# Optimization experiments

Hardware: AMD Instinct MI355X
Metric: run time of the kernel (lower is better)

Reference implementation:

```python
import jax, jax.numpy as jnp
import numpy as np

N, E, G = 100000, 400000, 2000
F_IN, HID, H = 74, 64, 4
HID4 = HID * H           # 256, per-node feature after flatten(1)
POOL = 3 * HID4          # 768, concat(mean, max, sum)
OUT = 128
NEG_SLOPE = 0.2          # DGL GATConv default LeakyReLU slope


def setup_inputs() -> dict:
    key = jax.random.key(0)
    ks = jax.random.split(key, 20)
    p = lambda k, shape: (jax.random.normal(k, shape, jnp.float32) * 0.05)
    inp = {
        "node_feat": jax.random.normal(ks[0], (N, F_IN), jnp.float32),
        "src": jax.random.randint(ks[1], (E,), 0, N, jnp.int32),
        "dst": jax.random.randint(ks[2], (E,), 0, N, jnp.int32),
        # every graph gets exactly N//G nodes (sorted, non-empty segments)
        "graph_ids": jnp.arange(N, dtype=jnp.int32) // (N // G),
        "enc_W": p(ks[3], (F_IN, HID)), "enc_b": jnp.zeros((HID,), jnp.float32),
    }
    in_dims = [HID, HID4, HID4]
    for l in range(3):
        inp[f"W{l}"] = p(ks[4 + 4 * l], (in_dims[l], H * HID))
        inp[f"al{l}"] = p(ks[5 + 4 * l], (H, HID))
        inp[f"ar{l}"] = p(ks[6 + 4 * l], (H, HID))
        inp[f"b{l}"] = jnp.zeros((H * HID,), jnp.float32)
    inp["r1_W"] = p(ks[16], (POOL, HID)); inp["r1_b"] = jnp.zeros((HID,), jnp.float32)
    inp["r2_W"] = p(ks[17], (HID, OUT)); inp["r2_b"] = jnp.zeros((OUT,), jnp.float32)
    return inp


def _gat_layer(h, src, dst, W, al, ar, b):
    # DGL GATConv (eval mode: dropouts are identity), activation=ReLU
    z = (h @ W).reshape(N, H, HID)                       # [N,H,O]
    el = jnp.einsum("nho,ho->nh", z, al)                 # [N,H]
    er = jnp.einsum("nho,ho->nh", z, ar)
    e = jax.nn.leaky_relu(el[src] + er[dst], NEG_SLOPE)  # [E,H]
    # segment softmax over incoming edges of each dst node, per head
    m = jax.ops.segment_max(e, dst, num_segments=N)      # [N,H]
    ex = jnp.exp(e - m[dst])
    s = jax.ops.segment_sum(ex, dst, num_segments=N)     # [N,H]
    a = ex / s[dst]                                      # [E,H]
    out = jax.ops.segment_sum(z[src] * a[:, :, None], dst, num_segments=N)
    out = out + b.reshape(1, H, HID)                     # GATConv bias
    return jax.nn.relu(out).reshape(N, HID4)             # flatten(1)


def reference(node_feat, src, dst, graph_ids, enc_W, enc_b,
              W0, al0, ar0, b0, W1, al1, ar1, b1, W2, al2, ar2, b2,
              r1_W, r1_b, r2_W, r2_b):
    h = node_feat @ enc_W + enc_b                        # node encoder
    h = _gat_layer(h, src, dst, W0, al0, ar0, b0)
    h = _gat_layer(h, src, dst, W1, al1, ar1, b1)
    h = _gat_layer(h, src, dst, W2, al2, ar2, b2)
    # multi-pool readout: mean / max / sum over nodes of each graph
    h_sum = jax.ops.segment_sum(h, graph_ids, num_segments=G)
    cnt = jax.ops.segment_sum(jnp.ones((N, 1), h.dtype), graph_ids, num_segments=G)
    h_mean = h_sum / cnt
    h_max = jax.ops.segment_max(h, graph_ids, num_segments=G)
    hg = jnp.concatenate([h_mean, h_max, h_sum], axis=1)  # [G, 3*HID4]
    hg = jax.nn.relu(hg @ r1_W + r1_b)
    return hg @ r2_W + r2_b                              # [G, OUT]
```

## Files before the change

kernel.cpp:

```cpp
#include <hip/hip_runtime.h>

#define N_NODES 100000
#define N_EDGES 400000
#define N_GRAPHS 2000
#define F_IN 74
#define ENC_KP 96
#define HID 64
#define NHEAD 4
#define HID4 256
#define OUT_DIM 128
#define NODES_PER_G 50

typedef __attribute__((ext_vector_type(8))) short short8;
typedef __attribute__((ext_vector_type(4))) float f32x4;

__device__ inline ushort f2bf(float f) {
  union { float f; unsigned u; } v; v.f = f;
  unsigned u = v.u;
  return (ushort)((u + 0x7FFFu + ((u >> 16) & 1u)) >> 16);
}
__device__ inline float bf2f(ushort b) {
  union { unsigned u; float f; } v; v.u = ((unsigned)b) << 16;
  return v.f;
}
__device__ inline float leaky(float x) { return x >= 0.f ? x : 0.2f * x; }

__device__ inline void glds16(const ushort* g, ushort* l) {
  __builtin_amdgcn_global_load_lds(
      (const __attribute__((address_space(1))) void*)g,
      (__attribute__((address_space(3))) void*)l, 16, 0, 0);
}

__global__ __launch_bounds__(256) void k_count(const int* __restrict__ dst,
                                               int* __restrict__ off) {
  int e = blockIdx.x * 256 + threadIdx.x;
  if (e < N_EDGES) atomicAdd(&off[dst[e] + 1], 1);
}

__global__ __launch_bounds__(256) void k_scan1(int* __restrict__ data, int n,
                                               int* __restrict__ blksum) {
  __shared__ int sh[256];
  int t = threadIdx.x;
  int base = blockIdx.x * 1024 + t * 4;
  int v0 = (base + 0 < n) ? data[base + 0] : 0;
  int v1 = (base + 1 < n) ? data[base + 1] : 0;
  int v2 = (base + 2 < n) ? data[base + 2] : 0;
  int v3 = (base + 3 < n) ? data[base + 3] : 0;
  v1 += v0; v2 += v1; v3 += v2;
  int tot = v3;
  sh[t] = tot;
  __syncthreads();
  for (int o = 1; o < 256; o <<= 1) {
    int x = (t >= o) ? sh[t - o] : 0;
    __syncthreads();
    sh[t] += x;
    __syncthreads();
  }
  int excl = sh[t] - tot;
  if (base + 0 < n) data[base + 0] = v0 + excl;
  if (base + 1 < n) data[base + 1] = v1 + excl;
  if (base + 2 < n) data[base + 2] = v2 + excl;
  if (base + 3 < n) data[base + 3] = v3 + excl;
  if (t == 255) blksum[blockIdx.x] = sh[255];
}

__global__ __launch_bounds__(256) void k_scan2(int* __restrict__ blksum, int nb) {
  __shared__ int sh[256];
  int t = threadIdx.x;
  sh[t] = (t < nb) ? blksum[t] : 0;
  __syncthreads();
  for (int o = 1; o < 256; o <<= 1) {
    int x = (t >= o) ? sh[t - o] : 0;
    __syncthreads();
    sh[t] += x;
    __syncthreads();
  }
  if (t < nb) blksum[t] = sh[t];
}

__global__ __launch_bounds__(256) void k_scan3(int* __restrict__ data, int n,
                                               const int* __restrict__ blksum) {
  int b = blockIdx.x;
  if (b == 0) return;
  int add = blksum[b - 1];
  int base = b * 1024 + threadIdx.x * 4;
  for (int j = 0; j < 4; ++j)
    if (base + j < n) data[base + j] += add;
}

__global__ __launch_bounds__(256) void k_scatter(const int* __restrict__ dst,
                                                 const int* __restrict__ src,
                                                 const int* __restrict__ off,
                                                 int* __restrict__ cursor,
                                                 int* __restrict__ srcs) {
  int e = blockIdx.x * 256 + threadIdx.x;
  if (e >= N_EDGES) return;
  int d = dst[e];
  int pos = off[d] + atomicAdd(&cursor[d], 1);
  srcs[pos] = src[e];
}

__global__ __launch_bounds__(256) void k_sortseg(const int* __restrict__ off,
                                                 int* __restrict__ srcs) {
  int n = blockIdx.x * 256 + threadIdx.x;
  if (n >= N_NODES) return;
  int beg = off[n], end = off[n + 1];
  for (int i = beg + 1; i < end; ++i) {
    int key = srcs[i];
    int j = i - 1;
    while (j >= beg && srcs[j] > key) { srcs[j + 1] = srcs[j]; --j; }
    srcs[j + 1] = key;
  }
}

__global__ __launch_bounds__(256) void k_pad_nf(const float* __restrict__ nf,
                                                ushort* __restrict__ nfb) {
  long long idx = (long long)blockIdx.x * 256 + threadIdx.x;
  if (idx >= (long long)N_NODES * ENC_KP) return;
  int n = (int)(idx / ENC_KP);
  int c = (int)(idx - (long long)n * ENC_KP);
  ushort v = 0;
  if (c < F_IN) v = f2bf(nf[(size_t)n * F_IN + c]);
  nfb[idx] = v;
}

__global__ __launch_bounds__(256) void k_wt_enc(const float* __restrict__ W,
                                                ushort* __restrict__ Wte) {
  int idx = blockIdx.x * 256 + threadIdx.x;
  if (idx >= HID * ENC_KP) return;
  int col = idx / ENC_KP;
  int k = idx - col * ENC_KP;
  ushort v = 0;
  if (k < F_IN) v = f2bf(W[(size_t)k * HID + col]);
  Wte[idx] = v;
}

__global__ __launch_bounds__(256) void k_enc_mfma(const ushort* __restrict__ A,
                                                  const ushort* __restrict__ Bt,
                                                  const float* __restrict__ bias,
                                                  ushort* __restrict__ Cb) {
  __shared__ ushort As[128][104];
  __shared__ ushort Bs[64][104];
  int t = threadIdx.x;
  int lane = t & 63;
  int wid = t >> 6;
  int brow = blockIdx.x * 128;

  {
    int r = t >> 1;
    int o = (t & 1) * 48;
    int gr = brow + r;
    const ushort* srcp = A + (size_t)gr * ENC_KP + o;
#pragma unroll
    for (int i = 0; i < 6; ++i) {
      int4 v = make_int4(0, 0, 0, 0);
      if (gr < N_NODES) v = *(const int4*)(srcp + i * 8);
      *(int4*)&As[r][o + i * 8] = v;
    }
  }
  if (t < 128) {
    int r = t >> 1;
    int o = (t & 1) * 48;
#pragma unroll
    for (int i = 0; i < 6; ++i)
      *(int4*)&Bs[r][o + i * 8] = *(const int4*)(Bt + (size_t)r * ENC_KP + o + i * 8);
  }
  __syncthreads();

  int fr = lane & 15;
  int ko = (lane >> 4) * 8;
  f32x4 acc[2][4];
#pragma unroll
  for (int m = 0; m < 2; ++m)
#pragma unroll
    for (int n = 0; n < 4; ++n) acc[m][n] = (f32x4)(0.f);

#pragma unroll
  for (int ks = 0; ks < 3; ++ks) {
    short8 a[2], b[4];
#pragma unroll
    for (int m = 0; m < 2; ++m) a[m] = *(const short8*)&As[wid * 32 + m * 16 + fr][ks * 32 + ko];
#pragma unroll
    for (int n = 0; n < 4; ++n) b[n] = *(const short8*)&Bs[n * 16 + fr][ks * 32 + ko];
#pragma unroll
    for (int m = 0; m < 2; ++m)
#pragma unroll
      for (int n = 0; n < 4; ++n)
        acc[m][n] = __builtin_amdgcn_mfma_f32_16x16x32_bf16(a[m], b[n], acc[m][n], 0, 0, 0);
  }

  int r0 = (lane >> 4) * 4;
  int cc = lane & 15;
#pragma unroll
  for (int m = 0; m < 2; ++m) {
#pragma unroll
    for (int j = 0; j < 4; ++j) {
      int row = brow + wid * 32 + m * 16 + r0 + j;
      if (row >= N_NODES) continue;
#pragma unroll
      for (int n = 0; n < 4; ++n) {
        int col = n * 16 + cc;
        Cb[(size_t)row * HID + col] = f2bf(acc[m][n][j] + bias[col]);
      }
    }
  }
}

template <int K>
__global__ __launch_bounds__(256) void k_wt(const float* __restrict__ W,
                                            ushort* __restrict__ Wt) {
  int idx = blockIdx.x * 256 + threadIdx.x;
  if (idx >= K * HID4) return;
  int k = idx >> 8;
  int n = idx & 255;
  Wt[(size_t)n * K + k] = f2bf(W[idx]);
}

template <int K>
__global__ __launch_bounds__(256) void k_gemm_mfma(const ushort* __restrict__ A,
                                                   const ushort* __restrict__ Bt,
                                                   ushort* __restrict__ Cb,
                                                   const float* __restrict__ al,
                                                   const float* __restrict__ ar,
                                                   float* __restrict__ el,
                                                   float* __restrict__ er,
                                                   int n_rows) {
  __shared__ __align__(16) ushort As[128 * 32];
  __shared__ __align__(16) ushort Bs[128 * 32];
  int t = threadIdx.x;
  int lane = t & 63;
  int wid = t >> 6;
  int wr = wid >> 1, wc = wid & 1;
  int brow = blockIdx.x * 128;
  int bcol = blockIdx.y * 128;

  f32x4 acc[4][4];
#pragma unroll
  for (int m = 0; m < 4; ++m)
#pragma unroll
    for (int n = 0; n < 4; ++n) acc[m][n] = (f32x4)(0.f);

  int srow0 = (wid * 2 + 0) * 16 + (lane >> 2);
  int srow1 = (wid * 2 + 1) * 16 + (lane >> 2);
  int skc = (lane & 3) * 8;
  int ga0 = brow + srow0; if (ga0 > n_rows - 1) ga0 = n_rows - 1;
  int ga1 = brow + srow1; if (ga1 > n_rows - 1) ga1 = n_rows - 1;
  const ushort* pa0 = A + (size_t)ga0 * K + skc;
  const ushort* pa1 = A + (size_t)ga1 * K + skc;
  const ushort* pb0 = Bt + (size_t)(bcol + srow0) * K + skc;
  const ushort* pb1 = Bt + (size_t)(bcol + srow1) * K + skc;
  ushort* la0 = As + (wid * 2 + 0) * 512;
  ushort* la1 = As + (wid * 2 + 1) * 512;
  ushort* lb0 = Bs + (wid * 2 + 0) * 512;
  ushort* lb1 = Bs + (wid * 2 + 1) * 512;

  int fr = lane & 15;
  int ko = (lane >> 4) * 8;

  for (int k0 = 0; k0 < K; k0 += 32) {
    glds16(pa0 + k0, la0);
    glds16(pa1 + k0, la1);
    glds16(pb0 + k0, lb0);
    glds16(pb1 + k0, lb1);
    __syncthreads();
    short8 a[4], b[4];
#pragma unroll
    for (int m = 0; m < 4; ++m)
      a[m] = *(const short8*)(As + (wr * 64 + m * 16 + fr) * 32 + ko);
#pragma unroll
    for (int n = 0; n < 4; ++n)
      b[n] = *(const short8*)(Bs + (wc * 64 + n * 16 + fr) * 32 + ko);
#pragma unroll
    for (int m = 0; m < 4; ++m)
#pragma unroll
      for (int n = 0; n < 4; ++n)
        acc[m][n] = __builtin_amdgcn_mfma_f32_16x16x32_bf16(a[m], b[n], acc[m][n], 0, 0, 0);
    __syncthreads();
  }

  int r0 = (lane >> 4) * 4;
  int cc = lane & 15;
  int q = blockIdx.y * 2 + wc;
  float alr[4], arr[4];
#pragma unroll
  for (int n = 0; n < 4; ++n) {
    int col = bcol + wc * 64 + n * 16 + cc;
    alr[n] = al[col];
    arr[n] = ar[col];
  }
#pragma unroll
  for (int m = 0; m < 4; ++m) {
#pragma unroll
    for (int j = 0; j < 4; ++j) {
      float pl = 0.f, pr = 0.f;
#pragma unroll
      for (int n = 0; n < 4; ++n) {
        pl = fmaf(acc[m][n][j], alr[n], pl);
        pr = fmaf(acc[m][n][j], arr[n], pr);
      }
#pragma unroll
      for (int o = 1; o < 16; o <<= 1) {
        pl += __shfl_xor(pl, o, 64);
        pr += __shfl_xor(pr, o, 64);
      }
      int row = brow + wr * 64 + m * 16 + r0 + j;
      if (row >= n_rows) continue;
      if (cc == 0) {
        el[(size_t)row * NHEAD + q] = pl;
        er[(size_t)row * NHEAD + q] = pr;
      }
#pragma unroll
      for (int n = 0; n < 4; ++n)
        Cb[(size_t)row * HID4 + bcol + wc * 64 + n * 16 + cc] = f2bf(acc[m][n][j]);
    }
  }
}

__global__ __launch_bounds__(256) void k_agg(const ushort* __restrict__ zb,
                                             const float* __restrict__ el,
                                             const float* __restrict__ er,
                                             const int* __restrict__ off,
                                             const int* __restrict__ srcs,
                                             const float* __restrict__ bias,
                                             ushort* __restrict__ outb) {
  int w = (blockIdx.x * 256 + threadIdx.x) >> 6;
  int lane = threadIdx.x & 63;
  int half = lane >> 5;
  int li = lane & 31;
  int n = w * 2 + half;
  if (n >= N_NODES) return;
  int h = li >> 3;
  int c = li * 8;
  int beg = off[n], end = off[n + 1];
  float erh = er[(size_t)n * NHEAD + h];

  float s = 0.f;
  float acc[8] = {0.f, 0.f, 0.f, 0.f, 0.f, 0.f, 0.f, 0.f};

  float e0 = 0.f, e1 = 0.f, e2 = 0.f;
  int4 z0 = make_int4(0, 0, 0, 0), z1 = z0, z2 = z0;
  if (beg < end) {
    int sn = srcs[beg];
    e0 = el[(size_t)sn * NHEAD + h];
    z0 = *(const int4*)(zb + (size_t)sn * HID4 + c);
  }
  if (beg + 1 < end) {
    int sn = srcs[beg + 1];
    e1 = el[(size_t)sn * NHEAD + h];
    z1 = *(const int4*)(zb + (size_t)sn * HID4 + c);
  }
  if (beg + 2 < end) {
    int sn = srcs[beg + 2];
    e2 = el[(size_t)sn * NHEAD + h];
    z2 = *(const int4*)(zb + (size_t)sn * HID4 + c);
  }
  for (int p = beg; p < end; ++p) {
    float ev = e0;
    int4 zv = z0;
    e0 = e1; z0 = z1;
    e1 = e2; z1 = z2;
    if (p + 3 < end) {
      int sn = srcs[p + 3];
      e2 = el[(size_t)sn * NHEAD + h];
      z2 = *(const int4*)(zb + (size_t)sn * HID4 + c);
    }
    float pv = __expf(leaky(ev + erh));
    s += pv;
    const ushort* us = (const ushort*)&zv;
#pragma unroll
    for (int j = 0; j < 8; ++j) acc[j] = fmaf(pv, bf2f(us[j]), acc[j]);
  }
  float inv = (s > 0.f) ? 1.f / s : 0.f;
  float4 b40 = *(const float4*)(bias + c);
  float4 b41 = *(const float4*)(bias + c + 4);
  float bb[8] = {b40.x, b40.y, b40.z, b40.w, b41.x, b41.y, b41.z, b41.w};
  int4 ov;
  ushort* os = (ushort*)&ov;
#pragma unroll
  for (int j = 0; j < 8; ++j) os[j] = f2bf(fmaxf(acc[j] * inv + bb[j], 0.f));
  *(int4*)(outb + (size_t)n * HID4 + c) = ov;
}

__global__ __launch_bounds__(256) void k_pool_mlp(const ushort* __restrict__ h,
                                                  const float* __restrict__ r1W,
                                                  const float* __restrict__ r1b,
                                                  const float* __restrict__ r2W,
                                                  const float* __restrict__ r2b,
                                                  float* __restrict__ out) {
  __shared__ float pooled[3 * HID4];
  __shared__ float part[4][HID];
  __shared__ float mid[HID];
  int g = blockIdx.x;
  int t = threadIdx.x;
  const ushort* base = h + (size_t)g * NODES_PER_G * HID4;
  float sum = 0.f, mx = -1e30f;
  for (int i = 0; i < NODES_PER_G; ++i) {
    float v = bf2f(base[(size_t)i * HID4 + t]);
    sum += v;
    mx = fmaxf(mx, v);
  }
  pooled[t] = sum / (float)NODES_PER_G;
  pooled[HID4 + t] = mx;
  pooled[2 * HID4 + t] = sum;
  __syncthreads();
  {
    int o = t & 63, chunk = t >> 6;
    float acc = 0.f;
    int k0 = chunk * 192;
    for (int k = k0; k < k0 + 192; ++k) acc = fmaf(pooled[k], r1W[k * HID + o], acc);
    part[chunk][o] = acc;
  }
  __syncthreads();
  if (t < HID) {
    float acc = r1b[t] + part[0][t] + part[1][t] + part[2][t] + part[3][t];
    mid[t] = fmaxf(acc, 0.f);
  }
  __syncthreads();
  if (t < OUT_DIM) {
    float acc = r2b[t];
    for (int k = 0; k < HID; ++k) acc = fmaf(mid[k], r2W[k * OUT_DIM + t], acc);
    out[(size_t)g * OUT_DIM + t] = acc;
  }
}

extern "C" void kernel_launch(void* const* d_in, const int* in_sizes, int n_in,
                              void* d_out, int out_size, void* d_ws, size_t ws_size,
                              hipStream_t stream) {
  const float* node_feat = (const float*)d_in[0];
  const int* src = (const int*)d_in[1];
  const int* dst = (const int*)d_in[2];
  const float* enc_W = (const float*)d_in[4];
  const float* enc_b = (const float*)d_in[5];
  const float* Wl[3] = {(const float*)d_in[6], (const float*)d_in[10], (const float*)d_in[14]};
  const float* all[3] = {(const float*)d_in[7], (const float*)d_in[11], (const float*)d_in[15]};
  const float* arl[3] = {(const float*)d_in[8], (const float*)d_in[12], (const float*)d_in[16]};
  const float* bl[3] = {(const float*)d_in[9], (const float*)d_in[13], (const float*)d_in[17]};
  const float* r1W = (const float*)d_in[18];
  const float* r1b = (const float*)d_in[19];
  const float* r2W = (const float*)d_in[20];
  const float* r2b = (const float*)d_in[21];
  float* out = (float*)d_out;

  char* p = (char*)d_ws;
  auto alloc = [&](size_t bytes) {
    void* r = (void*)p;
    p += (bytes + 255) & ~(size_t)255;
    return r;
  };
  int* off = (int*)alloc((N_NODES + 1) * sizeof(int));
  int* cursor = (int*)alloc(N_NODES * sizeof(int));
  int* srcs = (int*)alloc(N_EDGES * sizeof(int));
  int* blksum = (int*)alloc(256 * sizeof(int));
  float* el = (float*)alloc((size_t)N_NODES * NHEAD * sizeof(float));
  float* er = (float*)alloc((size_t)N_NODES * NHEAD * sizeof(float));
  ushort* Qb = (ushort*)alloc((size_t)N_NODES * HID4 * sizeof(ushort));
  ushort* Pb = (ushort*)alloc((size_t)N_NODES * HID4 * sizeof(ushort));
  ushort* Wt = (ushort*)alloc((size_t)HID4 * HID4 * sizeof(ushort));
  ushort* nfb = (ushort*)alloc((size_t)N_NODES * ENC_KP * sizeof(ushort));
  ushort* Wte = (ushort*)alloc((size_t)HID * ENC_KP * sizeof(ushort));

  hipMemsetAsync(off, 0, (N_NODES + 1) * sizeof(int), stream);
  hipMemsetAsync(cursor, 0, N_NODES * sizeof(int), stream);
  k_count<<<(N_EDGES + 255) / 256, 256, 0, stream>>>(dst, off);
  const int SCAN_N = N_NODES + 1;
  const int NB = (SCAN_N + 1023) / 1024;
  k_scan1<<<NB, 256, 0, stream>>>(off, SCAN_N, blksum);
  k_scan2<<<1, 256, 0, stream>>>(blksum, NB);
  k_scan3<<<NB, 256, 0, stream>>>(off, SCAN_N, blksum);
  k_scatter<<<(N_EDGES + 255) / 256, 256, 0, stream>>>(dst, src, off, cursor, srcs);
  k_sortseg<<<(N_NODES + 255) / 256, 256, 0, stream>>>(off, srcs);

  k_pad_nf<<<(int)(((long long)N_NODES * ENC_KP + 255) / 256), 256, 0, stream>>>(node_feat, nfb);
  k_wt_enc<<<(HID * ENC_KP + 255) / 256, 256, 0, stream>>>(enc_W, Wte);
  k_enc_mfma<<<(N_NODES + 127) / 128, 256, 0, stream>>>(nfb, Wte, enc_b, Pb);

  dim3 ggrid((N_NODES + 127) / 128, HID4 / 128);
  const int AGG_WAVES = (N_NODES + 1) / 2;
  const int AGG_BLOCKS = (AGG_WAVES + 3) / 4;
  for (int l = 0; l < 3; ++l) {
    if (l == 0) {
      k_wt<HID><<<(HID * HID4 + 255) / 256, 256, 0, stream>>>(Wl[0], Wt);
      k_gemm_mfma<HID><<<ggrid, 256, 0, stream>>>(Pb, Wt, Qb, all[0], arl[0], el, er, N_NODES);
    } else {
      k_wt<HID4><<<(HID4 * HID4 + 255) / 256, 256, 0, stream>>>(Wl[l], Wt);
      k_gemm_mfma<HID4><<<ggrid, 256, 0, stream>>>(Pb, Wt, Qb, all[l], arl[l], el, er, N_NODES);
    }
    k_agg<<<AGG_BLOCKS, 256, 0, stream>>>(Qb, el, er, off, srcs, bl[l], Pb);
  }

  k_pool_mlp<<<N_GRAPHS, 256, 0, stream>>>(Pb, r1W, r1b, r2W, r2b, out);
}
```

Before: 376.0 us.

## Fuse feature padding into encoder, double-buffer GEMM LDS, prefetch edge indices

```diff
diff --git a/kernel.cpp b/kernel.cpp
--- a/kernel.cpp
+++ b/kernel.cpp
@@ -113,17 +113,6 @@
   }
 }
 
-__global__ __launch_bounds__(256) void k_pad_nf(const float* __restrict__ nf,
-                                                ushort* __restrict__ nfb) {
-  long long idx = (long long)blockIdx.x * 256 + threadIdx.x;
-  if (idx >= (long long)N_NODES * ENC_KP) return;
-  int n = (int)(idx / ENC_KP);
-  int c = (int)(idx - (long long)n * ENC_KP);
-  ushort v = 0;
-  if (c < F_IN) v = f2bf(nf[(size_t)n * F_IN + c]);
-  nfb[idx] = v;
-}
-
 __global__ __launch_bounds__(256) void k_wt_enc(const float* __restrict__ W,
                                                 ushort* __restrict__ Wte) {
   int idx = blockIdx.x * 256 + threadIdx.x;
@@ -135,7 +124,7 @@
   Wte[idx] = v;
 }
 
-__global__ __launch_bounds__(256) void k_enc_mfma(const ushort* __restrict__ A,
+__global__ __launch_bounds__(256) void k_enc_mfma(const float* __restrict__ nf,
                                                   const ushort* __restrict__ Bt,
                                                   const float* __restrict__ bias,
                                                   ushort* __restrict__ Cb) {
@@ -146,17 +135,13 @@
   int wid = t >> 6;
   int brow = blockIdx.x * 128;
 
-  {
-    int r = t >> 1;
-    int o = (t & 1) * 48;
+  for (int i = t; i < 128 * ENC_KP; i += 256) {
+    int r = i / ENC_KP;
+    int c = i - r * ENC_KP;
     int gr = brow + r;
-    const ushort* srcp = A + (size_t)gr * ENC_KP + o;
-#pragma unroll
-    for (int i = 0; i < 6; ++i) {
-      int4 v = make_int4(0, 0, 0, 0);
-      if (gr < N_NODES) v = *(const int4*)(srcp + i * 8);
-      *(int4*)&As[r][o + i * 8] = v;
-    }
+    float v = 0.f;
+    if (gr < N_NODES && c < F_IN) v = nf[(size_t)gr * F_IN + c];
+    As[r][c] = f2bf(v);
   }
   if (t < 128) {
     int r = t >> 1;
@@ -225,8 +210,8 @@
                                                    float* __restrict__ el,
                                                    float* __restrict__ er,
                                                    int n_rows) {
-  __shared__ __align__(16) ushort As[128 * 32];
-  __shared__ __align__(16) ushort Bs[128 * 32];
+  __shared__ __align__(16) ushort As[2][128 * 32];
+  __shared__ __align__(16) ushort Bs[2][128 * 32];
   int t = threadIdx.x;
   int lane = t & 63;
   int wid = t >> 6;
@@ -249,33 +234,40 @@
   const ushort* pa1 = A + (size_t)ga1 * K + skc;
   const ushort* pb0 = Bt + (size_t)(bcol + srow0) * K + skc;
   const ushort* pb1 = Bt + (size_t)(bcol + srow1) * K + skc;
-  ushort* la0 = As + (wid * 2 + 0) * 512;
-  ushort* la1 = As + (wid * 2 + 1) * 512;
-  ushort* lb0 = Bs + (wid * 2 + 0) * 512;
-  ushort* lb1 = Bs + (wid * 2 + 1) * 512;
+  int lo0 = (wid * 2 + 0) * 512;
+  int lo1 = (wid * 2 + 1) * 512;
 
   int fr = lane & 15;
   int ko = (lane >> 4) * 8;
 
+  glds16(pa0, &As[0][lo0]);
+  glds16(pa1, &As[0][lo1]);
+  glds16(pb0, &Bs[0][lo0]);
+  glds16(pb1, &Bs[0][lo1]);
+  __syncthreads();
+  int cur = 0;
+
   for (int k0 = 0; k0 < K; k0 += 32) {
-    glds16(pa0 + k0, la0);
-    glds16(pa1 + k0, la1);
-    glds16(pb0 + k0, lb0);
-    glds16(pb1 + k0, lb1);
-    __syncthreads();
+    if (k0 + 32 < K) {
+      glds16(pa0 + k0 + 32, &As[cur ^ 1][lo0]);
+      glds16(pa1 + k0 + 32, &As[cur ^ 1][lo1]);
+      glds16(pb0 + k0 + 32, &Bs[cur ^ 1][lo0]);
+      glds16(pb1 + k0 + 32, &Bs[cur ^ 1][lo1]);
+    }
     short8 a[4], b[4];
 #pragma unroll
     for (int m = 0; m < 4; ++m)
-      a[m] = *(const short8*)(As + (wr * 64 + m * 16 + fr) * 32 + ko);
+      a[m] = *(const short8*)(&As[cur][0] + (wr * 64 + m * 16 + fr) * 32 + ko);
 #pragma unroll
     for (int n = 0; n < 4; ++n)
-      b[n] = *(const short8*)(Bs + (wc * 64 + n * 16 + fr) * 32 + ko);
+      b[n] = *(const short8*)(&Bs[cur][0] + (wc * 64 + n * 16 + fr) * 32 + ko);
 #pragma unroll
     for (int m = 0; m < 4; ++m)
 #pragma unroll
       for (int n = 0; n < 4; ++n)
         acc[m][n] = __builtin_amdgcn_mfma_f32_16x16x32_bf16(a[m], b[n], acc[m][n], 0, 0, 0);
     __syncthreads();
+    cur ^= 1;
   }
 
   int r0 = (lane >> 4) * 4;
@@ -354,16 +346,21 @@
     e2 = el[(size_t)sn * NHEAD + h];
     z2 = *(const int4*)(zb + (size_t)sn * HID4 + c);
   }
+  int sn3 = (beg + 3 < end) ? srcs[beg + 3] : 0;
+
   for (int p = beg; p < end; ++p) {
     float ev = e0;
     int4 zv = z0;
     e0 = e1; z0 = z1;
     e1 = e2; z1 = z2;
+    int sn4 = (p + 4 < end) ? srcs[p + 4] : 0;
     if (p + 3 < end) {
-      int sn = srcs[p + 3];
-      e2 = el[(size_t)sn * NHEAD + h];
-      z2 = *(const int4*)(zb + (size_t)sn * HID4 + c);
+      e2 = el[(size_t)sn3 * NHEAD + h];
+      z2 = *(const int4*)(zb + (size_t)sn3 * HID4 + c);
+    } else {
+      e2 = 0.f;
     }
+    sn3 = sn4;
     float pv = __expf(leaky(ev + erh));
     s += pv;
     const ushort* us = (const ushort*)&zv;
@@ -456,7 +453,6 @@
   ushort* Qb = (ushort*)alloc((size_t)N_NODES * HID4 * sizeof(ushort));
   ushort* Pb = (ushort*)alloc((size_t)N_NODES * HID4 * sizeof(ushort));
   ushort* Wt = (ushort*)alloc((size_t)HID4 * HID4 * sizeof(ushort));
-  ushort* nfb = (ushort*)alloc((size_t)N_NODES * ENC_KP * sizeof(ushort));
   ushort* Wte = (ushort*)alloc((size_t)HID * ENC_KP * sizeof(ushort));
 
   hipMemsetAsync(off, 0, (N_NODES + 1) * sizeof(int), stream);
@@ -470,9 +466,8 @@
   k_scatter<<<(N_EDGES + 255) / 256, 256, 0, stream>>>(dst, src, off, cursor, srcs);
   k_sortseg<<<(N_NODES + 255) / 256, 256, 0, stream>>>(off, srcs);
 
-  k_pad_nf<<<(int)(((long long)N_NODES * ENC_KP + 255) / 256), 256, 0, stream>>>(node_feat, nfb);
   k_wt_enc<<<(HID * ENC_KP + 255) / 256, 256, 0, stream>>>(enc_W, Wte);
-  k_enc_mfma<<<(N_NODES + 127) / 128, 256, 0, stream>>>(nfb, Wte, enc_b, Pb);
+  k_enc_mfma<<<(N_NODES + 127) / 128, 256, 0, stream>>>(node_feat, Wte, enc_b, Pb);
 
   dim3 ggrid((N_NODES + 127) / 128, HID4 / 128);
   const int AGG_WAVES = (N_NODES + 1) / 2;
```

New measurement: 378.9 us. About the same (+0.8%).
